# Performance work log

Measured on AMD Instinct MI355X. Metric: run time of the kernel, lower is better.

The kernel has to match this reference:

```python
import jax, jax.numpy as jnp
import numpy as np
from jax import lax

B, CIN, N = 4, 3, 2048
H, COUT, LEVELS = 128, 3, 3
HEADS = 8

# jnp.convolve(x, f, 'same') with len(f)=8 == correlation with f[::-1], x zero-padded (4,3).
# DWT then takes [::2], which is conv stride 2. IDWT zero-upsamples (lhs_dilation=2) then
# convolves 'same' with f[::-1], i.e. correlation with f, padding (4,4).

def _dwt(x, wlow, whigh):
    # x: (M, L) -> approx, detail each (M, L//2)
    rhs = jnp.stack([wlow[::-1], whigh[::-1]])[:, None, :]  # (2,1,8)
    out = lax.conv_general_dilated(x[:, None, :], rhs, window_strides=(2,),
                                   padding=[(4, 3)],
                                   dimension_numbers=('NCH', 'OIH', 'NCH'))
    return out[:, 0, :], out[:, 1, :]

def _idwt(a, d, wlow, whigh):
    # a, d: (M, L) -> (M, 2L); recon_low + recon_high fused as a 2-in-channel conv
    lhs = jnp.stack([a, d], axis=1)               # (M,2,L)
    rhs = jnp.stack([wlow, whigh])[None, :, :]    # (1,2,8)
    out = lax.conv_general_dilated(lhs, rhs, window_strides=(1,),
                                   padding=[(4, 4)], lhs_dilation=(2,),
                                   dimension_numbers=('NCH', 'OIH', 'NCH'))
    return out[:, 0, :]


def setup_inputs() -> dict:
    key = jax.random.key(0)
    ks = jax.random.split(key, 12)
    db4_low = jnp.array([0.23037781, 0.71484657, 0.63088076, -0.02798376,
                         -0.18703481, 0.03084138, 0.03288301, -0.0105974], jnp.float32)
    db4_high = jnp.array([-0.0105974, -0.03288301, 0.03084138, 0.18703481,
                          -0.02798376, -0.63088076, 0.71484657, -0.23037781], jnp.float32)
    def s(k, shape, fan_in):
        return jax.random.normal(k, shape, jnp.float32) * (1.0 / fan_in) ** 0.5
    return {
        'x': jax.random.normal(ks[0], (B, CIN, N), jnp.float32),
        'wlow': db4_low, 'whigh': db4_high,
        'Win': s(ks[1], (CIN, H), CIN), 'b_in': jnp.zeros((H,), jnp.float32),
        'W1': s(ks[2], (LEVELS, 2, 2 * H), 2), 'b1': jnp.zeros((LEVELS, 2 * H), jnp.float32),
        'W2': s(ks[3], (LEVELS, 2 * H, H), 2 * H), 'b2': jnp.zeros((LEVELS, H), jnp.float32),
        'Wq': s(ks[4], (H, H), H), 'bq': jnp.zeros((H,), jnp.float32),
        'Wk': s(ks[5], (H, H), H), 'bk': jnp.zeros((H,), jnp.float32),
        'Wv': s(ks[6], (H, H), H), 'bv': jnp.zeros((H,), jnp.float32),
        'Wo': s(ks[7], (H, H), H), 'bo': jnp.zeros((H,), jnp.float32),
        'Wout': s(ks[8], (H, COUT), H), 'bout': jnp.zeros((COUT,), jnp.float32),
    }


def reference(x, wlow, whigh, Win, b_in, W1, b1, W2, b2,
              Wq, bq, Wk, bk, Wv, bv, Wo, bo, Wout, bout):
    Bx = x.shape[0]
    # input projection: (B,CIN,N) -> (B,H,N)
    xp = jnp.einsum('bcn,ch->bhn', x, Win) + b_in[None, :, None]
    cur = xp.reshape(Bx * H, N)  # per-(batch,channel) 1D signals, fully batched
    proc = []  # processed coeffs per level; note approx == detail after the shared mean
    for lvl in range(LEVELS):
        a, d = _dwt(cur, wlow, whigh)                 # (M, L)
        c = jnp.stack([a, d], axis=-1)                # (M, L, 2)
        h = jax.nn.gelu(c @ W1[lvl] + b1[lvl])        # (M, L, 2H)
        p = (h @ W2[lvl] + b2[lvl]).mean(axis=-1)     # (M, L): mean over hidden dim
        proc.append(p)
        cur = a
    rec = proc[-1]  # start from deepest processed approx
    for lvl in range(LEVELS - 1, -1, -1):
        rec = _idwt(rec, proc[lvl], wlow, whigh)
    y = rec.reshape(Bx, H, N)
    # cross-level attention: standard MHA with embed_dim=H, 8 heads, no dropout
    seq = y.transpose(0, 2, 1)  # (B,N,H)
    dh = H // HEADS
    q = (seq @ Wq + bq).reshape(Bx, N, HEADS, dh)
    k = (seq @ Wk + bk).reshape(Bx, N, HEADS, dh)
    v = (seq @ Wv + bv).reshape(Bx, N, HEADS, dh)
    att = jnp.einsum('bqhd,bkhd->bhqk', q, k) * (dh ** -0.5)
    att = jax.nn.softmax(att, axis=-1)
    o = jnp.einsum('bhqk,bkhd->bqhd', att, v).reshape(Bx, N, H)
    o = o @ Wo + bo
    out = o @ Wout + bout  # (B,N,COUT)
    return out.transpose(0, 2, 1)  # (B,COUT,N)
```

## Files before the change

### kernel.cpp

```cpp
#include <hip/hip_runtime.h>

#define N_    2048
#define H_    128
#define B_    4
#define CIN_  3
#define COUT_ 3
#define LOG2E 1.44269504089f

__device__ __forceinline__ float gelu_tanh(float x) {
    float x2 = x * x;
    float e = __builtin_amdgcn_exp2f(x * fmaf(-0.10294340397f, x2, -2.30220899f));
    return x * __builtin_amdgcn_rcpf(1.0f + e);
}

__global__ void prep_kernel(const float* __restrict__ W2, const float* __restrict__ b2,
                            const float* __restrict__ Wo, const float* __restrict__ bo,
                            const float* __restrict__ Wout, const float* __restrict__ bout,
                            float* __restrict__ w2m, float* __restrict__ b2m,
                            float* __restrict__ wf, float* __restrict__ bf) {
    int gid = blockIdx.x * 256 + threadIdx.x;
    if (gid < 768) {
        const float* r = W2 + (size_t)gid * 128;
        float s = 0.f;
        for (int h = 0; h < 128; ++h) s += r[h];
        w2m[gid] = s * (1.0f / 128.0f);
    } else if (gid < 771) {
        int lvl = gid - 768;
        const float* r = b2 + lvl * 128;
        float s = 0.f;
        for (int h = 0; h < 128; ++h) s += r[h];
        b2m[lvl] = s * (1.0f / 128.0f);
    } else if (gid >= 1024 && gid < 1408) {
        int e = gid - 1024;
        int h = e / 3, c = e - 3 * h;
        float s = 0.f;
        for (int j = 0; j < 128; ++j) s = fmaf(Wo[h * 128 + j], Wout[j * 3 + c], s);
        wf[e] = s;
    } else if (gid >= 1408 && gid < 1411) {
        int c = gid - 1408;
        float s = bout[c];
        for (int j = 0; j < 128; ++j) s = fmaf(bo[j], Wout[j * 3 + c], s);
        bf[c] = s;
    }
}

template<bool FUSEX>
__global__ __launch_bounds__(256) void dwt_mlp_kernel(
        const float* __restrict__ src, int loSh,
        const float* __restrict__ x, const float* __restrict__ Win,
        const float* __restrict__ b_in,
        const float* __restrict__ wlow, const float* __restrict__ whigh,
        const float* __restrict__ W1l, const float* __restrict__ b1l,
        const float* __restrict__ w2ml, const float* __restrict__ b2ml,
        float* __restrict__ a_out, float* __restrict__ p_out) {
    __shared__ float4 wp[256];
    __shared__ float wls[8], whs[8];
    int tid = threadIdx.x;
    wp[tid] = make_float4(W1l[tid], W1l[256 + tid], b1l[tid], w2ml[tid]);
    if (tid < 8) { wls[tid] = wlow[tid]; whs[tid] = whigh[tid]; }
    __syncthreads();

    int gid = blockIdx.x * 256 + tid;
    int Lo  = 1 << loSh;
    int m   = gid >> loSh;
    int i   = gid & (Lo - 1);
    int L   = Lo << 1;
    int j0  = 2 * i - 4;
    float xw[8];
    if (FUSEX) {
        int b = m >> 7, h = m & 127;
        float w0 = Win[h], w1 = Win[128 + h], w2 = Win[256 + h];
        float bi = b_in[h];
        const float* xr = x + (size_t)b * (CIN_ * N_);
#pragma unroll
        for (int t = 0; t < 8; ++t) {
            int j = j0 + t;
            bool ok = (unsigned)j < (unsigned)L;
            int jc = ok ? j : 0;
            float v = bi;
            v = fmaf(xr[jc], w0, v);
            v = fmaf(xr[N_ + jc], w1, v);
            v = fmaf(xr[2 * N_ + jc], w2, v);
            xw[t] = ok ? v : 0.f;
        }
    } else {
        const float* row = src + (size_t)m * L;
#pragma unroll
        for (int t = 0; t < 8; ++t) {
            int j = j0 + t;
            xw[t] = ((unsigned)j < (unsigned)L) ? row[j] : 0.f;
        }
    }
    float a = 0.f, d = 0.f;
#pragma unroll
    for (int t = 0; t < 8; ++t) {
        a = fmaf(xw[t], wls[7 - t], a);
        d = fmaf(xw[t], whs[7 - t], d);
    }
    float acc = 0.f;
#pragma unroll 8
    for (int kk = 0; kk < 256; ++kk) {
        float4 w = wp[kk];
        float t = fmaf(a, w.x, fmaf(d, w.y, w.z));
        acc = fmaf(gelu_tanh(t), w.w, acc);
    }
    a_out[gid] = a;
    p_out[gid] = acc + b2ml[0];
}

__global__ __launch_bounds__(256) void idwt_kernel(
        const float* __restrict__ aSrc, const float* __restrict__ dSrc,
        int loutSh, const float* __restrict__ wlow, const float* __restrict__ whigh,
        float* __restrict__ out) {
    __shared__ float wls[8], whs[8];
    int tid = threadIdx.x;
    if (tid < 8) { wls[tid] = wlow[tid]; whs[tid] = whigh[tid]; }
    __syncthreads();
    int gid  = blockIdx.x * 256 + tid;
    int Lout = 1 << loutSh;
    int L    = Lout >> 1;
    int m    = gid >> loutSh;
    int ii   = gid & (Lout - 1);
    const float* ar = aSrc + (size_t)m * L;
    const float* dr = dSrc + (size_t)m * L;
    int podd = ii & 1;
    int off0 = (ii >> 1) - 2 + podd;
    float r = 0.f;
#pragma unroll
    for (int s = 0; s < 4; ++s) {
        int idx = off0 + s;
        bool ok = (unsigned)idx < (unsigned)L;
        float av = ok ? ar[idx] : 0.f;
        float dv = ok ? dr[idx] : 0.f;
        r = fmaf(av, wls[2 * s + podd], r);
        r = fmaf(dv, whs[2 * s + podd], r);
    }
    out[gid] = r;
}

__global__ __launch_bounds__(384) void qkv_kernel(
        const float* __restrict__ r0,
        const float* __restrict__ Wq, const float* __restrict__ bq,
        const float* __restrict__ Wk, const float* __restrict__ bk,
        const float* __restrict__ Wv, const float* __restrict__ bv,
        float* __restrict__ qB, float* __restrict__ kB, float* __restrict__ vB) {
    __shared__ float As[16 * 130];
    int tid = threadIdx.x;
    int rowbase = blockIdx.x * 16;
    int b  = rowbase >> 11;
    int n0 = rowbase & 2047;
    for (int idx = tid; idx < 2048; idx += 384) {
        int h = idx >> 4;
        int r = idx & 15;
        As[r * 130 + h] = r0[((size_t)(b * H_ + h)) * N_ + n0 + r];
    }
    __syncthreads();

    const float* W; const float* bias; float* dst; int jj;
    if (tid < 128)      { W = Wq; bias = bq; dst = qB; jj = tid; }
    else if (tid < 256) { W = Wk; bias = bk; dst = kB; jj = tid - 128; }
    else                { W = Wv; bias = bv; dst = vB; jj = tid - 256; }

    float acc[16];
#pragma unroll
    for (int r = 0; r < 16; ++r) acc[r] = 0.f;
    for (int h = 0; h < 128; ++h) {
        float w = W[h * 128 + jj];
#pragma unroll
        for (int r = 0; r < 16; ++r) acc[r] = fmaf(As[r * 130 + h], w, acc[r]);
    }
    float bb = bias[jj];
    int head = jj >> 4, t = jj & 15;
    size_t obase = ((size_t)(b * 8 + head) * N_) * 16 + t;
#pragma unroll
    for (int r = 0; r < 16; ++r)
        dst[obase + (size_t)(n0 + r) * 16] = acc[r] + bb;
}

#define DOT4(acc, qq, aa) do { acc = fmaf(qq.x, aa.x, acc); acc = fmaf(qq.y, aa.y, acc); \
                               acc = fmaf(qq.z, aa.z, acc); acc = fmaf(qq.w, aa.w, acc); } while (0)
#define SCALE4(oo, c)     do { oo.x *= c; oo.y *= c; oo.z *= c; oo.w *= c; } while (0)
#define AXPY4(oo, p, aa)  do { oo.x = fmaf(p, aa.x, oo.x); oo.y = fmaf(p, aa.y, oo.y); \
                               oo.z = fmaf(p, aa.z, oo.z); oo.w = fmaf(p, aa.w, oo.w); } while (0)

template<int KS>
__global__ __launch_bounds__(128, 4) void attn_kernel(
        const float* __restrict__ qb, const float* __restrict__ kb,
        const float* __restrict__ vb,
        float* __restrict__ part_o, float* __restrict__ part_ml) {
    __shared__ float4 kt4[512];
    __shared__ float4 vt4[512];
    int tid   = threadIdx.x;
    int blk   = blockIdx.x;
    int split = blk % KS;
    int qblk  = (blk / KS) & 7;
    int bh    = blk / (8 * KS);
    int nA    = qblk * 256 + tid;
    int nB    = nA + 128;

    const float4* ksrc = (const float4*)(kb + (size_t)bh * (N_ * 16));
    const float4* vsrc = (const float4*)(vb + (size_t)bh * (N_ * 16));
    const float4* qra  = (const float4*)(qb + ((size_t)bh * N_ + nA) * 16);
    const float4* qrb  = (const float4*)(qb + ((size_t)bh * N_ + nB) * 16);
    const float sc = 0.25f * LOG2E;
    float4 qa0 = qra[0], qa1 = qra[1], qa2 = qra[2], qa3 = qra[3];
    float4 qb0 = qrb[0], qb1 = qrb[1], qb2 = qrb[2], qb3 = qrb[3];
    SCALE4(qa0, sc); SCALE4(qa1, sc); SCALE4(qa2, sc); SCALE4(qa3, sc);
    SCALE4(qb0, sc); SCALE4(qb1, sc); SCALE4(qb2, sc); SCALE4(qb3, sc);

    float mA = -3.0e38f, lA = 0.f, mB = -3.0e38f, lB = 0.f;
    float4 oA0 = {0,0,0,0}, oA1 = oA0, oA2 = oA0, oA3 = oA0;
    float4 oB0 = oA0, oB1 = oA0, oB2 = oA0, oB3 = oA0;

    int k0 = split * (N_ / KS);
    for (int t0 = k0; t0 < k0 + N_ / KS; t0 += 128) {
        __syncthreads();
        const float4* ks = ksrc + t0 * 4;
        const float4* vs = vsrc + t0 * 4;
        kt4[tid] = ks[tid]; kt4[tid+128] = ks[tid+128]; kt4[tid+256] = ks[tid+256]; kt4[tid+384] = ks[tid+384];
        vt4[tid] = vs[tid]; vt4[tid+128] = vs[tid+128]; vt4[tid+256] = vs[tid+256]; vt4[tid+384] = vs[tid+384];
        __syncthreads();

        for (int c0 = 0; c0 < 128; c0 += 8) {
            float svA[8], svB[8];
            float cmA = -3.0e38f, cmB = -3.0e38f;
#pragma unroll
            for (int c = 0; c < 8; ++c) {
                int kr = (c0 + c) * 4;
                float4 k0v = kt4[kr], k1v = kt4[kr+1], k2v = kt4[kr+2], k3v = kt4[kr+3];
                float s0 = 0.f, s1 = 0.f, u0 = 0.f, u1 = 0.f;
                DOT4(s0, qa0, k0v); DOT4(s1, qa1, k1v); DOT4(s0, qa2, k2v); DOT4(s1, qa3, k3v);
                DOT4(u0, qb0, k0v); DOT4(u1, qb1, k1v); DOT4(u0, qb2, k2v); DOT4(u1, qb3, k3v);
                svA[c] = s0 + s1; svB[c] = u0 + u1;
                cmA = fmaxf(cmA, svA[c]); cmB = fmaxf(cmB, svB[c]);
            }
            if (__any((cmA > mA + 8.f) || (cmB > mB + 8.f))) {
                float mnA = fmaxf(mA, cmA), mnB = fmaxf(mB, cmB);
                float cA = __builtin_amdgcn_exp2f(mA - mnA);
                float cB = __builtin_amdgcn_exp2f(mB - mnB);
                lA *= cA; lB *= cB;
                SCALE4(oA0, cA); SCALE4(oA1, cA); SCALE4(oA2, cA); SCALE4(oA3, cA);
                SCALE4(oB0, cB); SCALE4(oB1, cB); SCALE4(oB2, cB); SCALE4(oB3, cB);
                mA = mnA; mB = mnB;
            }
#pragma unroll
            for (int c = 0; c < 8; ++c) {
                float pA = __builtin_amdgcn_exp2f(svA[c] - mA);
                float pB = __builtin_amdgcn_exp2f(svB[c] - mB);
                lA += pA; lB += pB;
                int vr = (c0 + c) * 4;
                float4 v0 = vt4[vr], v1 = vt4[vr+1], v2 = vt4[vr+2], v3 = vt4[vr+3];
                AXPY4(oA0, pA, v0); AXPY4(oA1, pA, v1); AXPY4(oA2, pA, v2); AXPY4(oA3, pA, v3);
                AXPY4(oB0, pB, v0); AXPY4(oB1, pB, v1); AXPY4(oB2, pB, v2); AXPY4(oB3, pB, v3);
            }
        }
    }
    int qgA = bh * N_ + nA, qgB = bh * N_ + nB;
    float4* poA = (float4*)part_o + ((size_t)split * 65536 + qgA) * 4;
    poA[0] = oA0; poA[1] = oA1; poA[2] = oA2; poA[3] = oA3;
    float4* poB = (float4*)part_o + ((size_t)split * 65536 + qgB) * 4;
    poB[0] = oB0; poB[1] = oB1; poB[2] = oB2; poB[3] = oB3;
    ((float2*)part_ml)[(size_t)split * 65536 + qgA] = make_float2(mA, lA);
    ((float2*)part_ml)[(size_t)split * 65536 + qgB] = make_float2(mB, lB);
}

template<int KS>
__global__ __launch_bounds__(512) void combine_final_kernel(
        const float* __restrict__ part_o, const float* __restrict__ part_ml,
        const float* __restrict__ wf, const float* __restrict__ bf,
        float* __restrict__ out) {
    __shared__ float ysh[64 * 129];
    __shared__ float wfs[384];
    __shared__ float bfs[3];
    int tid = threadIdx.x;
    if (tid < 384) wfs[tid] = wf[tid];
    if (tid >= 384 && tid < 387) bfs[tid - 384] = bf[tid - 384];
    int b = blockIdx.x >> 5, nb = blockIdx.x & 31;
    int head = tid >> 6, nl = tid & 63;
    int n = nb * 64 + nl;
    int qg = (b * 8 + head) * N_ + n;

    float m[KS], l[KS];
    float M = -3.0e38f;
#pragma unroll
    for (int s = 0; s < KS; ++s) {
        float2 ml = ((const float2*)part_ml)[(size_t)s * 65536 + qg];
        m[s] = ml.x; l[s] = ml.y;
        M = fmaxf(M, m[s]);
    }
    float w[KS], lt = 0.f;
#pragma unroll
    for (int s = 0; s < KS; ++s) {
        w[s] = __builtin_amdgcn_exp2f(m[s] - M);
        lt = fmaf(l[s], w[s], lt);
    }
    float inv = __builtin_amdgcn_rcpf(lt);
    float o[16];
#pragma unroll
    for (int j = 0; j < 16; ++j) o[j] = 0.f;
#pragma unroll
    for (int s = 0; s < KS; ++s) {
        const float4* po = (const float4*)part_o + ((size_t)s * 65536 + qg) * 4;
#pragma unroll
        for (int r = 0; r < 4; ++r) {
            float4 v = po[r];
            o[4*r+0] = fmaf(v.x, w[s], o[4*r+0]);
            o[4*r+1] = fmaf(v.y, w[s], o[4*r+1]);
            o[4*r+2] = fmaf(v.z, w[s], o[4*r+2]);
            o[4*r+3] = fmaf(v.w, w[s], o[4*r+3]);
        }
    }
    int col = head * 16;
#pragma unroll
    for (int j = 0; j < 16; ++j) ysh[nl * 129 + col + j] = o[j] * inv;
    __syncthreads();
    if (tid < 192) {
        int c = tid >> 6, nl2 = tid & 63;
        float acc = bfs[c];
        const float* yr = ysh + nl2 * 129;
#pragma unroll 4
        for (int h = 0; h < 128; ++h) acc = fmaf(yr[h], wfs[h * 3 + c], acc);
        out[((size_t)b * 3 + c) * N_ + nb * 64 + nl2] = acc;
    }
}

extern "C" void kernel_launch(void* const* d_in, const int* in_sizes, int n_in,
                              void* d_out, int out_size, void* d_ws, size_t ws_size,
                              hipStream_t stream) {
    const float* x    = (const float*)d_in[0];
    const float* wlow = (const float*)d_in[1];
    const float* whigh= (const float*)d_in[2];
    const float* Win  = (const float*)d_in[3];
    const float* b_in = (const float*)d_in[4];
    const float* W1   = (const float*)d_in[5];
    const float* b1   = (const float*)d_in[6];
    const float* W2   = (const float*)d_in[7];
    const float* b2   = (const float*)d_in[8];
    const float* Wq   = (const float*)d_in[9];
    const float* bq   = (const float*)d_in[10];
    const float* Wk   = (const float*)d_in[11];
    const float* bk   = (const float*)d_in[12];
    const float* Wv   = (const float*)d_in[13];
    const float* bv   = (const float*)d_in[14];
    const float* Wo   = (const float*)d_in[15];
    const float* bo   = (const float*)d_in[16];
    const float* Wout = (const float*)d_in[17];
    const float* bout = (const float*)d_in[18];
    float* out = (float*)d_out;
    (void)in_sizes; (void)n_in; (void)out_size;

    float* ws = (float*)d_ws;
    float* qBuf  = ws;
    float* kBuf  = ws + 1048576;
    float* vBuf  = ws + 2097152;
    float* base2 = ws + 3145728;
    float* a1 = base2;
    float* p0 = base2 + 524288;
    float* a2 = base2 + 1048576;
    float* p1 = base2 + 1310720;
    float* a3 = base2 + 1572864;
    float* p2 = base2 + 1703936;
    float* r2 = base2 + 1835008;
    float* r1 = base2 + 2097152;
    float* r0 = base2 + 2621440;

    const size_t need8 = (3145728ull + 8ull * 1048576 + 8ull * 131072 + 2048ull) * 4;
    int KS = (ws_size >= need8) ? 8 : 4;

    float* part_o  = base2;
    float* part_ml = base2 + (size_t)KS * 1048576;
    float* smalls  = part_ml + (size_t)KS * 131072;
    float* w2m = smalls;
    float* b2m = smalls + 768;
    float* wf  = smalls + 771;
    float* bf  = smalls + 1155;

    prep_kernel<<<8, 256, 0, stream>>>(W2, b2, Wo, bo, Wout, bout, w2m, b2m, wf, bf);

    dwt_mlp_kernel<true><<<2048, 256, 0, stream>>>(nullptr, 10, x, Win, b_in, wlow, whigh,
                                                   W1 + 0,    b1 + 0,   w2m + 0,   b2m + 0, a1, p0);
    dwt_mlp_kernel<false><<<1024, 256, 0, stream>>>(a1, 9, nullptr, nullptr, nullptr, wlow, whigh,
                                                    W1 + 512,  b1 + 256, w2m + 256, b2m + 1, a2, p1);
    dwt_mlp_kernel<false><<<512, 256, 0, stream>>>(a2, 8, nullptr, nullptr, nullptr, wlow, whigh,
                                                   W1 + 1024, b1 + 512, w2m + 512, b2m + 2, a3, p2);

    idwt_kernel<<<1024, 256, 0, stream>>>(p2, p2, 9,  wlow, whigh, r2);
    idwt_kernel<<<2048, 256, 0, stream>>>(r2, p1, 10, wlow, whigh, r1);
    idwt_kernel<<<4096, 256, 0, stream>>>(r1, p0, 11, wlow, whigh, r0);

    qkv_kernel<<<512, 384, 0, stream>>>(r0, Wq, bq, Wk, bk, Wv, bv, qBuf, kBuf, vBuf);

    if (KS == 8) {
        attn_kernel<8><<<32 * 8 * 8, 128, 0, stream>>>(qBuf, kBuf, vBuf, part_o, part_ml);
        combine_final_kernel<8><<<128, 512, 0, stream>>>(part_o, part_ml, wf, bf, out);
    } else {
        attn_kernel<4><<<32 * 8 * 4, 128, 0, stream>>>(qBuf, kBuf, vBuf, part_o, part_ml);
        combine_final_kernel<4><<<128, 512, 0, stream>>>(part_o, part_ml, wf, bf, out);
    }
}
```

Baseline: 372.2 us.

## Raise attention query tile to four per thread and drop LDS staging elsewhere

The attention kernel now processes four queries per thread instead of two, halving the grid and relaxing launch bounds to 2 waves, so each K/V tile loaded into shared memory is reused across more queries. It also packs the MLP weights into a float4 buffer in the prep kernel, and replaces shared-memory staging in the DWT, IDWT, QKV and combine kernels with direct global reads. The wider attention tile raises register pressure and occupancy drops. The QKV kernel loses its transposed LDS tile and now reads strided rows from global memory.

```diff
diff --git a/kernel.cpp b/kernel.cpp
--- a/kernel.cpp
+++ b/kernel.cpp
@@ -13,17 +13,20 @@
     return x * __builtin_amdgcn_rcpf(1.0f + e);
 }
 
-__global__ void prep_kernel(const float* __restrict__ W2, const float* __restrict__ b2,
+__global__ void prep_kernel(const float* __restrict__ W1, const float* __restrict__ b1,
+                            const float* __restrict__ W2, const float* __restrict__ b2,
                             const float* __restrict__ Wo, const float* __restrict__ bo,
                             const float* __restrict__ Wout, const float* __restrict__ bout,
-                            float* __restrict__ w2m, float* __restrict__ b2m,
+                            float4* __restrict__ wpack, float* __restrict__ b2m,
                             float* __restrict__ wf, float* __restrict__ bf) {
     int gid = blockIdx.x * 256 + threadIdx.x;
     if (gid < 768) {
         const float* r = W2 + (size_t)gid * 128;
         float s = 0.f;
         for (int h = 0; h < 128; ++h) s += r[h];
-        w2m[gid] = s * (1.0f / 128.0f);
+        int lvl = gid >> 8, k = gid & 255;
+        wpack[gid] = make_float4(W1[lvl * 512 + k], W1[lvl * 512 + 256 + k],
+                                 b1[gid], s * (1.0f / 128.0f));
     } else if (gid < 771) {
         int lvl = gid - 768;
         const float* r = b2 + lvl * 128;
@@ -50,16 +53,9 @@
         const float* __restrict__ x, const float* __restrict__ Win,
         const float* __restrict__ b_in,
         const float* __restrict__ wlow, const float* __restrict__ whigh,
-        const float* __restrict__ W1l, const float* __restrict__ b1l,
-        const float* __restrict__ w2ml, const float* __restrict__ b2ml,
+        const float4* __restrict__ wpack, const float* __restrict__ b2ml,
         float* __restrict__ a_out, float* __restrict__ p_out) {
-    __shared__ float4 wp[256];
-    __shared__ float wls[8], whs[8];
     int tid = threadIdx.x;
-    wp[tid] = make_float4(W1l[tid], W1l[256 + tid], b1l[tid], w2ml[tid]);
-    if (tid < 8) { wls[tid] = wlow[tid]; whs[tid] = whigh[tid]; }
-    __syncthreads();
-
     int gid = blockIdx.x * 256 + tid;
     int Lo  = 1 << loSh;
     int m   = gid >> loSh;
@@ -94,13 +90,13 @@
     float a = 0.f, d = 0.f;
 #pragma unroll
     for (int t = 0; t < 8; ++t) {
-        a = fmaf(xw[t], wls[7 - t], a);
-        d = fmaf(xw[t], whs[7 - t], d);
+        a = fmaf(xw[t], wlow[7 - t], a);
+        d = fmaf(xw[t], whigh[7 - t], d);
     }
     float acc = 0.f;
 #pragma unroll 8
     for (int kk = 0; kk < 256; ++kk) {
-        float4 w = wp[kk];
+        float4 w = wpack[kk];
         float t = fmaf(a, w.x, fmaf(d, w.y, w.z));
         acc = fmaf(gelu_tanh(t), w.w, acc);
     }
@@ -112,10 +108,7 @@
         const float* __restrict__ aSrc, const float* __restrict__ dSrc,
         int loutSh, const float* __restrict__ wlow, const float* __restrict__ whigh,
         float* __restrict__ out) {
-    __shared__ float wls[8], whs[8];
-    int tid = threadIdx.x;
-    if (tid < 8) { wls[tid] = wlow[tid]; whs[tid] = whigh[tid]; }
-    __syncthreads();
+    int tid  = threadIdx.x;
     int gid  = blockIdx.x * 256 + tid;
     int Lout = 1 << loutSh;
     int L    = Lout >> 1;
@@ -125,6 +118,12 @@
     const float* dr = dSrc + (size_t)m * L;
     int podd = ii & 1;
     int off0 = (ii >> 1) - 2 + podd;
+    float wlp[4], whp[4];
+#pragma unroll
+    for (int s = 0; s < 4; ++s) {
+        wlp[s] = podd ? wlow[2 * s + 1] : wlow[2 * s];
+        whp[s] = podd ? whigh[2 * s + 1] : whigh[2 * s];
+    }
     float r = 0.f;
 #pragma unroll
     for (int s = 0; s < 4; ++s) {
@@ -132,8 +131,8 @@
         bool ok = (unsigned)idx < (unsigned)L;
         float av = ok ? ar[idx] : 0.f;
         float dv = ok ? dr[idx] : 0.f;
-        r = fmaf(av, wls[2 * s + podd], r);
-        r = fmaf(dv, whs[2 * s + podd], r);
+        r = fmaf(av, wlp[s], r);
+        r = fmaf(dv, whp[s], r);
     }
     out[gid] = r;
 }
@@ -144,30 +143,25 @@
         const float* __restrict__ Wk, const float* __restrict__ bk,
         const float* __restrict__ Wv, const float* __restrict__ bv,
         float* __restrict__ qB, float* __restrict__ kB, float* __restrict__ vB) {
-    __shared__ float As[16 * 130];
     int tid = threadIdx.x;
     int rowbase = blockIdx.x * 16;
     int b  = rowbase >> 11;
     int n0 = rowbase & 2047;
-    for (int idx = tid; idx < 2048; idx += 384) {
-        int h = idx >> 4;
-        int r = idx & 15;
-        As[r * 130 + h] = r0[((size_t)(b * H_ + h)) * N_ + n0 + r];
-    }
-    __syncthreads();
 
     const float* W; const float* bias; float* dst; int jj;
     if (tid < 128)      { W = Wq; bias = bq; dst = qB; jj = tid; }
     else if (tid < 256) { W = Wk; bias = bk; dst = kB; jj = tid - 128; }
     else                { W = Wv; bias = bv; dst = vB; jj = tid - 256; }
 
+    const float* abase = r0 + (size_t)b * (H_ * N_) + n0;
     float acc[16];
 #pragma unroll
     for (int r = 0; r < 16; ++r) acc[r] = 0.f;
     for (int h = 0; h < 128; ++h) {
         float w = W[h * 128 + jj];
-#pragma unroll
-        for (int r = 0; r < 16; ++r) acc[r] = fmaf(As[r * 130 + h], w, acc[r]);
+        const float* ar = abase + (size_t)h * N_;
+#pragma unroll
+        for (int r = 0; r < 16; ++r) acc[r] = fmaf(ar[r], w, acc[r]);
     }
     float bb = bias[jj];
     int head = jj >> 4, t = jj & 15;
@@ -184,7 +178,7 @@
                                oo.z = fmaf(p, aa.z, oo.z); oo.w = fmaf(p, aa.w, oo.w); } while (0)
 
 template<int KS>
-__global__ __launch_bounds__(128, 4) void attn_kernel(
+__global__ __launch_bounds__(128, 2) void attn_kernel(
         const float* __restrict__ qb, const float* __restrict__ kb,
         const float* __restrict__ vb,
         float* __restrict__ part_o, float* __restrict__ part_ml) {
@@ -193,75 +187,88 @@
     int tid   = threadIdx.x;
     int blk   = blockIdx.x;
     int split = blk % KS;
-    int qblk  = (blk / KS) & 7;
-    int bh    = blk / (8 * KS);
-    int nA    = qblk * 256 + tid;
-    int nB    = nA + 128;
+    int qblk  = (blk / KS) & 3;
+    int bh    = blk / (4 * KS);
 
     const float4* ksrc = (const float4*)(kb + (size_t)bh * (N_ * 16));
     const float4* vsrc = (const float4*)(vb + (size_t)bh * (N_ * 16));
-    const float4* qra  = (const float4*)(qb + ((size_t)bh * N_ + nA) * 16);
-    const float4* qrb  = (const float4*)(qb + ((size_t)bh * N_ + nB) * 16);
     const float sc = 0.25f * LOG2E;
-    float4 qa0 = qra[0], qa1 = qra[1], qa2 = qra[2], qa3 = qra[3];
-    float4 qb0 = qrb[0], qb1 = qrb[1], qb2 = qrb[2], qb3 = qrb[3];
-    SCALE4(qa0, sc); SCALE4(qa1, sc); SCALE4(qa2, sc); SCALE4(qa3, sc);
-    SCALE4(qb0, sc); SCALE4(qb1, sc); SCALE4(qb2, sc); SCALE4(qb3, sc);
-
-    float mA = -3.0e38f, lA = 0.f, mB = -3.0e38f, lB = 0.f;
-    float4 oA0 = {0,0,0,0}, oA1 = oA0, oA2 = oA0, oA3 = oA0;
-    float4 oB0 = oA0, oB1 = oA0, oB2 = oA0, oB3 = oA0;
+
+    float4 q[4][4];
+    float  m[4], l[4];
+    float4 o[4][4];
+#pragma unroll
+    for (int qi = 0; qi < 4; ++qi) {
+        const float4* qr = (const float4*)(qb + ((size_t)bh * N_ + qblk * 512 + qi * 128 + tid) * 16);
+#pragma unroll
+        for (int j = 0; j < 4; ++j) { q[qi][j] = qr[j]; SCALE4(q[qi][j], sc); }
+        m[qi] = -3.0e38f; l[qi] = 0.f;
+#pragma unroll
+        for (int j = 0; j < 4; ++j) o[qi][j] = make_float4(0.f, 0.f, 0.f, 0.f);
+    }
 
     int k0 = split * (N_ / KS);
     for (int t0 = k0; t0 < k0 + N_ / KS; t0 += 128) {
         __syncthreads();
         const float4* ks = ksrc + t0 * 4;
         const float4* vs = vsrc + t0 * 4;
-        kt4[tid] = ks[tid]; kt4[tid+128] = ks[tid+128]; kt4[tid+256] = ks[tid+256]; kt4[tid+384] = ks[tid+384];
-        vt4[tid] = vs[tid]; vt4[tid+128] = vs[tid+128]; vt4[tid+256] = vs[tid+256]; vt4[tid+384] = vs[tid+384];
+#pragma unroll
+        for (int u = 0; u < 4; ++u) {
+            kt4[tid + u * 128] = ks[tid + u * 128];
+            vt4[tid + u * 128] = vs[tid + u * 128];
+        }
         __syncthreads();
 
-        for (int c0 = 0; c0 < 128; c0 += 8) {
-            float svA[8], svB[8];
-            float cmA = -3.0e38f, cmB = -3.0e38f;
-#pragma unroll
-            for (int c = 0; c < 8; ++c) {
+        for (int c0 = 0; c0 < 128; c0 += 4) {
+            float sv[4][4];
+            float cm[4] = {-3.0e38f, -3.0e38f, -3.0e38f, -3.0e38f};
+#pragma unroll
+            for (int c = 0; c < 4; ++c) {
                 int kr = (c0 + c) * 4;
                 float4 k0v = kt4[kr], k1v = kt4[kr+1], k2v = kt4[kr+2], k3v = kt4[kr+3];
-                float s0 = 0.f, s1 = 0.f, u0 = 0.f, u1 = 0.f;
-                DOT4(s0, qa0, k0v); DOT4(s1, qa1, k1v); DOT4(s0, qa2, k2v); DOT4(s1, qa3, k3v);
-                DOT4(u0, qb0, k0v); DOT4(u1, qb1, k1v); DOT4(u0, qb2, k2v); DOT4(u1, qb3, k3v);
-                svA[c] = s0 + s1; svB[c] = u0 + u1;
-                cmA = fmaxf(cmA, svA[c]); cmB = fmaxf(cmB, svB[c]);
+#pragma unroll
+                for (int qi = 0; qi < 4; ++qi) {
+                    float s0 = 0.f, s1 = 0.f;
+                    DOT4(s0, q[qi][0], k0v); DOT4(s1, q[qi][1], k1v);
+                    DOT4(s0, q[qi][2], k2v); DOT4(s1, q[qi][3], k3v);
+                    sv[qi][c] = s0 + s1;
+                    cm[qi] = fmaxf(cm[qi], sv[qi][c]);
+                }
             }
-            if (__any((cmA > mA + 8.f) || (cmB > mB + 8.f))) {
-                float mnA = fmaxf(mA, cmA), mnB = fmaxf(mB, cmB);
-                float cA = __builtin_amdgcn_exp2f(mA - mnA);
-                float cB = __builtin_amdgcn_exp2f(mB - mnB);
-                lA *= cA; lB *= cB;
-                SCALE4(oA0, cA); SCALE4(oA1, cA); SCALE4(oA2, cA); SCALE4(oA3, cA);
-                SCALE4(oB0, cB); SCALE4(oB1, cB); SCALE4(oB2, cB); SCALE4(oB3, cB);
-                mA = mnA; mB = mnB;
+            bool need = (cm[0] > m[0] + 8.f) || (cm[1] > m[1] + 8.f) ||
+                        (cm[2] > m[2] + 8.f) || (cm[3] > m[3] + 8.f);
+            if (__any(need)) {
+#pragma unroll
+                for (int qi = 0; qi < 4; ++qi) {
+                    float mn = fmaxf(m[qi], cm[qi]);
+                    float cr = __builtin_amdgcn_exp2f(m[qi] - mn);
+                    l[qi] *= cr;
+#pragma unroll
+                    for (int j = 0; j < 4; ++j) SCALE4(o[qi][j], cr);
+                    m[qi] = mn;
+                }
             }
 #pragma unroll
-            for (int c = 0; c < 8; ++c) {
-                float pA = __builtin_amdgcn_exp2f(svA[c] - mA);
-                float pB = __builtin_amdgcn_exp2f(svB[c] - mB);
-                lA += pA; lB += pB;
+            for (int c = 0; c < 4; ++c) {
                 int vr = (c0 + c) * 4;
                 float4 v0 = vt4[vr], v1 = vt4[vr+1], v2 = vt4[vr+2], v3 = vt4[vr+3];
-                AXPY4(oA0, pA, v0); AXPY4(oA1, pA, v1); AXPY4(oA2, pA, v2); AXPY4(oA3, pA, v3);
-                AXPY4(oB0, pB, v0); AXPY4(oB1, pB, v1); AXPY4(oB2, pB, v2); AXPY4(oB3, pB, v3);
+#pragma unroll
+                for (int qi = 0; qi < 4; ++qi) {
+                    float p = __builtin_amdgcn_exp2f(sv[qi][c] - m[qi]);
+                    l[qi] += p;
+                    AXPY4(o[qi][0], p, v0); AXPY4(o[qi][1], p, v1);
+                    AXPY4(o[qi][2], p, v2); AXPY4(o[qi][3], p, v3);
+                }
             }
         }
     }
-    int qgA = bh * N_ + nA, qgB = bh * N_ + nB;
-    float4* poA = (float4*)part_o + ((size_t)split * 65536 + qgA) * 4;
-    poA[0] = oA0; poA[1] = oA1; poA[2] = oA2; poA[3] = oA3;
-    float4* poB = (float4*)part_o + ((size_t)split * 65536 + qgB) * 4;
-    poB[0] = oB0; poB[1] = oB1; poB[2] = oB2; poB[3] = oB3;
-    ((float2*)part_ml)[(size_t)split * 65536 + qgA] = make_float2(mA, lA);
-    ((float2*)part_ml)[(size_t)split * 65536 + qgB] = make_float2(mB, lB);
+#pragma unroll
+    for (int qi = 0; qi < 4; ++qi) {
+        int qg = bh * N_ + qblk * 512 + qi * 128 + tid;
+        float4* po = (float4*)part_o + ((size_t)split * 65536 + qg) * 4;
+        po[0] = o[qi][0]; po[1] = o[qi][1]; po[2] = o[qi][2]; po[3] = o[qi][3];
+        ((float2*)part_ml)[(size_t)split * 65536 + qg] = make_float2(m[qi], l[qi]);
+    }
 }
 
 template<int KS>
@@ -270,11 +277,7 @@
         const float* __restrict__ wf, const float* __restrict__ bf,
         float* __restrict__ out) {
     __shared__ float ysh[64 * 129];
-    __shared__ float wfs[384];
-    __shared__ float bfs[3];
     int tid = threadIdx.x;
-    if (tid < 384) wfs[tid] = wf[tid];
-    if (tid >= 384 && tid < 387) bfs[tid - 384] = bf[tid - 384];
     int b = blockIdx.x >> 5, nb = blockIdx.x & 31;
     int head = tid >> 6, nl = tid & 63;
     int n = nb * 64 + nl;
@@ -316,10 +319,10 @@
     __syncthreads();
     if (tid < 192) {
         int c = tid >> 6, nl2 = tid & 63;
-        float acc = bfs[c];
+        float acc = bf[c];
         const float* yr = ysh + nl2 * 129;
 #pragma unroll 4
-        for (int h = 0; h < 128; ++h) acc = fmaf(yr[h], wfs[h * 3 + c], acc);
+        for (int h = 0; h < 128; ++h) acc = fmaf(yr[h], wf[h * 3 + c], acc);
         out[((size_t)b * 3 + c) * N_ + nb * 64 + nl2] = acc;
     }
 }
@@ -364,25 +367,25 @@
     float* r1 = base2 + 2097152;
     float* r0 = base2 + 2621440;
 
-    const size_t need8 = (3145728ull + 8ull * 1048576 + 8ull * 131072 + 2048ull) * 4;
+    const size_t need8 = (3145728ull + 8ull * 1048576 + 8ull * 131072 + 8192ull) * 4;
     int KS = (ws_size >= need8) ? 8 : 4;
 
     float* part_o  = base2;
     float* part_ml = base2 + (size_t)KS * 1048576;
     float* smalls  = part_ml + (size_t)KS * 131072;
-    float* w2m = smalls;
-    float* b2m = smalls + 768;
-    float* wf  = smalls + 771;
-    float* bf  = smalls + 1155;
-
-    prep_kernel<<<8, 256, 0, stream>>>(W2, b2, Wo, bo, Wout, bout, w2m, b2m, wf, bf);
+    float4* wpack = (float4*)smalls;
+    float* b2m = smalls + 3072;
+    float* wf  = smalls + 3088;
+    float* bf  = smalls + 3472;
+
+    prep_kernel<<<8, 256, 0, stream>>>(W1, b1, W2, b2, Wo, bo, Wout, bout, wpack, b2m, wf, bf);
 
     dwt_mlp_kernel<true><<<2048, 256, 0, stream>>>(nullptr, 10, x, Win, b_in, wlow, whigh,
-                                                   W1 + 0,    b1 + 0,   w2m + 0,   b2m + 0, a1, p0);
+                                                   wpack + 0,   b2m + 0, a1, p0);
     dwt_mlp_kernel<false><<<1024, 256, 0, stream>>>(a1, 9, nullptr, nullptr, nullptr, wlow, whigh,
-                                                    W1 + 512,  b1 + 256, w2m + 256, b2m + 1, a2, p1);
+                                                    wpack + 256, b2m + 1, a2, p1);
     dwt_mlp_kernel<false><<<512, 256, 0, stream>>>(a2, 8, nullptr, nullptr, nullptr, wlow, whigh,
-                                                   W1 + 1024, b1 + 512, w2m + 512, b2m + 2, a3, p2);
+                                                   wpack + 512, b2m + 2, a3, p2);
 
     idwt_kernel<<<1024, 256, 0, stream>>>(p2, p2, 9,  wlow, whigh, r2);
     idwt_kernel<<<2048, 256, 0, stream>>>(r2, p1, 10, wlow, whigh, r1);
@@ -391,10 +394,10 @@
     qkv_kernel<<<512, 384, 0, stream>>>(r0, Wq, bq, Wk, bk, Wv, bv, qBuf, kBuf, vBuf);
 
     if (KS == 8) {
-        attn_kernel<8><<<32 * 8 * 8, 128, 0, stream>>>(qBuf, kBuf, vBuf, part_o, part_ml);
+        attn_kernel<8><<<32 * 4 * 8, 128, 0, stream>>>(qBuf, kBuf, vBuf, part_o, part_ml);
         combine_final_kernel<8><<<128, 512, 0, stream>>>(part_o, part_ml, wf, bf, out);
     } else {
-        attn_kernel<4><<<32 * 8 * 4, 128, 0, stream>>>(qBuf, kBuf, vBuf, part_o, part_ml);
+        attn_kernel<4><<<32 * 4 * 4, 128, 0, stream>>>(qBuf, kBuf, vBuf, part_o, part_ml);
         combine_final_kernel<4><<<128, 512, 0, stream>>>(part_o, part_ml, wf, bf, out);
     }
 }
```

Measured after the change: 358.4 us. 1.04x faster.
